# Kernel tuning notes

Measured on AMD Instinct MI355X. Metric: run time of the kernel, lower is better.

The kernel has to match this reference:

```python
import jax, jax.numpy as jnp
import numpy as np

COMMITMENT_COST = 0.25


def setup_inputs() -> dict:
    key = jax.random.key(0)
    k1, k2 = jax.random.split(key)
    x = jax.random.normal(k1, (32, 256, 32, 32), dtype=jnp.float32)          # NCHW latents
    embedding = jax.random.normal(k2, (1024, 256), dtype=jnp.float32)        # [K, D] codebook
    return {"x": x, "embedding": embedding}


def reference(x, embedding):
    # NCHW -> NHWC, flatten to [N, D]
    inp = jnp.transpose(x, (0, 2, 3, 1))
    B, H, W, D = inp.shape
    K = embedding.shape[0]
    flat = inp.reshape(-1, D)                                                # [N, D]

    dists = (jnp.sum(flat * flat, axis=1, keepdims=True)
             + jnp.sum(embedding * embedding, axis=1)
             - 2.0 * flat @ embedding.T)
    idx = jnp.argmin(dists, axis=1)                                          # [N]
    encodings = jax.nn.one_hot(idx, K, dtype=flat.dtype)                     # [N, K]

    quantized = (encodings @ embedding).reshape(B, H, W, D)

    # commitment loss (codebook detached, eval path: no EMA update)
    e_latent_loss = jnp.mean(jnp.square(jax.lax.stop_gradient(quantized) - inp))
    loss = COMMITMENT_COST * e_latent_loss

    # straight-through estimator
    quantized_st = inp + jax.lax.stop_gradient(quantized - inp)

    avg_probs = jnp.mean(encodings, axis=0)
    perplexity = jnp.exp(-jnp.sum(avg_probs * jnp.log(avg_probs + 1e-10)))

    return (loss, jnp.transpose(quantized_st, (0, 3, 1, 2)), perplexity, encodings)
```

## Files before the change

### kernel.cpp

```cpp
#include <hip/hip_runtime.h>
#include <math.h>

#define D    256
#define K    1024
#define HWX  1024
#define NPTS 32768
#define PT   64
#define NPAIR 32

#define Q_OFF    1
#define PERP_OFF (1 + 8388608)
#define ENC_OFF  (2 + 8388608)

#define WS_FRAG_OFF 147456

typedef __attribute__((ext_vector_type(8))) short bf16x8;
typedef __attribute__((ext_vector_type(4))) float f32x4;
typedef __attribute__((ext_vector_type(2))) float f32x2;

__device__ __forceinline__ unsigned short bf16_rne(float f) {
  unsigned int u = __float_as_uint(f);
  u = u + 0x7fffu + ((u >> 16) & 1u);
  return (unsigned short)(u >> 16);
}

#define CONV(F, H, L)                                                          \
  {                                                                            \
    H = bf16_rne(F);                                                           \
    const float fh_ = __uint_as_float((unsigned)(H) << 16);                    \
    L = bf16_rne((F)-fh_);                                                     \
  }

__global__ __launch_bounds__(256) void vq_frag(const float* __restrict__ emb,
                                               unsigned int* __restrict__ frag,
                                               float* __restrict__ enorm,
                                               int* __restrict__ counts,
                                               float* __restrict__ loss_accum) {
  const int gid = blockIdx.x * 256 + threadIdx.x;
  const int c = gid >> 5, g = gid & 31;
  const float* src = emb + (size_t)c * D + g * 8;
  const float4 a = *(const float4*)src;
  const float4 b = *(const float4*)(src + 4);
  float s = a.x * a.x + a.y * a.y + a.z * a.z + a.w * a.w +
            b.x * b.x + b.y * b.y + b.z * b.z + b.w * b.w;
#pragma unroll
  for (int off = 1; off < 32; off <<= 1) s += __shfl_xor(s, off);
  if (g == 0) enorm[c] = s;
  unsigned short h0, h1, h2, h3, h4, h5, h6, h7;
  unsigned short l0, l1, l2, l3, l4, l5, l6, l7;
  CONV(a.x, h0, l0) CONV(a.y, h1, l1) CONV(a.z, h2, l2) CONV(a.w, h3, l3)
  CONV(b.x, h4, l4) CONV(b.y, h5, l5) CONV(b.z, h6, l6) CONV(b.w, h7, l7)
  uint4 uh, ul;
  uh.x = (unsigned)h0 | ((unsigned)h1 << 16); uh.y = (unsigned)h2 | ((unsigned)h3 << 16);
  uh.z = (unsigned)h4 | ((unsigned)h5 << 16); uh.w = (unsigned)h6 | ((unsigned)h7 << 16);
  ul.x = (unsigned)l0 | ((unsigned)l1 << 16); ul.y = (unsigned)l2 | ((unsigned)l3 << 16);
  ul.z = (unsigned)l4 | ((unsigned)l5 << 16); ul.w = (unsigned)l6 | ((unsigned)l7 << 16);
  const int fragidx = (c >> 4) * 16 + (g >> 2) * 2;
  const int Lo = ((c & 15) + 16 * (g & 3)) * 4;
  *(uint4*)(frag + (size_t)fragidx * 256 + Lo) = uh;
  *(uint4*)(frag + (size_t)(fragidx + 1) * 256 + Lo) = ul;
  if (gid < K) counts[gid] = 0;
  if (gid == 0) *loss_accum = 0.0f;
}

#define ISSUE_PAIR(P, HALF)                                                    \
  {                                                                            \
    const unsigned* gsrc = fragg + (size_t)(P)*8192 + t * 4;                   \
    unsigned short* ldst = fbuf + (HALF)*16384 + t * 8;                        \
    _Pragma("unroll") for (int q = 0; q < 8; ++q)                              \
        __builtin_amdgcn_global_load_lds(                                      \
            (const __attribute__((address_space(1))) unsigned*)(gsrc + q * 1024), \
            (__attribute__((address_space(3))) unsigned*)(ldst + q * 2048),    \
            16, 0, 0);                                                         \
  }

#define AHOIST(KSv)                                                            \
  ah##KSv = *(const bf16x8*)&fbuf[((w * 4 + ((KSv)&3)) * 2 + 0) * 512 + lane * 8]; \
  al##KSv = *(const bf16x8*)&fbuf[((w * 4 + ((KSv)&3)) * 2 + 1) * 512 + lane * 8];

#define KS3G(KSv, ACC, BUFO)                                                   \
  {                                                                            \
    const bf16x8 bh = *(const bf16x8*)&fbuf[(BUFO) + ((KSv)*2 + 0) * 512 + lane * 8]; \
    const bf16x8 bl = *(const bf16x8*)&fbuf[(BUFO) + ((KSv)*2 + 1) * 512 + lane * 8]; \
    ACC = __builtin_amdgcn_mfma_f32_16x16x32_bf16(ah##KSv, bh, ACC, 0, 0, 0);  \
    ACC = __builtin_amdgcn_mfma_f32_16x16x32_bf16(al##KSv, bh, ACC, 0, 0, 0);  \
    ACC = __builtin_amdgcn_mfma_f32_16x16x32_bf16(ah##KSv, bl, ACC, 0, 0, 0);  \
  }

#define COMPUTE_PAIR(I)                                                        \
  {                                                                            \
    const int b0 = ((I)&1) * 16384;                                            \
    const int b1 = b0 + 8192;                                                  \
    f32x4 acc0 = {0.f, 0.f, 0.f, 0.f};                                         \
    f32x4 acc1 = {0.f, 0.f, 0.f, 0.f};                                         \
    KS3G(0, acc0, b0) KS3G(0, acc1, b1)                                        \
    KS3G(1, acc0, b0) KS3G(1, acc1, b1)                                        \
    KS3G(2, acc0, b0) KS3G(2, acc1, b1)                                        \
    KS3G(3, acc0, b0) KS3G(3, acc1, b1)                                        \
    KS3G(4, acc0, b0) KS3G(4, acc1, b1)                                        \
    KS3G(5, acc0, b0) KS3G(5, acc1, b1)                                        \
    KS3G(6, acc0, b0) KS3G(6, acc1, b1)                                        \
    KS3G(7, acc0, b0) KS3G(7, acc1, b1)                                        \
    const int c0 = (I)*32 + (lane & 15);                                       \
    const int c1 = c0 + 16;                                                    \
    const float e0 = en_s[c0], e1 = en_s[c1];                                  \
    float m;                                                                   \
    m = e0 - 2.0f * acc0[0]; if (m < mv[0]) { mv[0] = m; mi[0] = c0; }         \
    m = e0 - 2.0f * acc0[1]; if (m < mv[1]) { mv[1] = m; mi[1] = c0; }         \
    m = e0 - 2.0f * acc0[2]; if (m < mv[2]) { mv[2] = m; mi[2] = c0; }         \
    m = e0 - 2.0f * acc0[3]; if (m < mv[3]) { mv[3] = m; mi[3] = c0; }         \
    m = e1 - 2.0f * acc1[0]; if (m < mv[0]) { mv[0] = m; mi[0] = c1; }         \
    m = e1 - 2.0f * acc1[1]; if (m < mv[1]) { mv[1] = m; mi[1] = c1; }         \
    m = e1 - 2.0f * acc1[2]; if (m < mv[2]) { mv[2] = m; mi[2] = c1; }         \
    m = e1 - 2.0f * acc1[3]; if (m < mv[3]) { mv[3] = m; mi[3] = c1; }         \
  }

#define ENC_ZERO2(I)                                                           \
  {                                                                            \
    const f32x2 z_ = {0.f, 0.f};                                               \
    __builtin_nontemporal_store(z_, encz + (I)*1024 + t);                      \
    __builtin_nontemporal_store(z_, encz + (I)*1024 + 256 + t);                \
    __builtin_nontemporal_store(z_, encz + (I)*1024 + 512 + t);                \
    __builtin_nontemporal_store(z_, encz + (I)*1024 + 768 + t);                \
  }

#define CFENCE asm volatile("" ::: "memory");

#define STAGE_X(H)                                                             \
  {                                                                            \
    const int pt = t & 63, cb_ = t >> 6;                                       \
    const float* xb = x + (size_t)bb * (D * HWX) + hw0 + pt;                   \
    _Pragma("unroll 8") for (int i = 0; i < 32; ++i) {                         \
      const int c = (H)*128 + cb_ + 4 * i;                                     \
      const float f = xb[(size_t)c * HWX];                                     \
      unsigned short h_, l_;                                                   \
      CONV(f, h_, l_)                                                          \
      xn_acc += f * f;                                                         \
      const int ksl = (c >> 5) & 3, quad = (c >> 3) & 3, j = c & 7;            \
      const int base =                                                         \
          (((pt >> 4) * 4 + ksl) * 2) * 512 + ((pt & 15) + 16 * quad) * 8 + j; \
      fbuf[base] = h_;                                                         \
      fbuf[base + 512] = l_;                                                   \
    }                                                                          \
  }

__global__ __launch_bounds__(256) void vq_main(const float* __restrict__ x,
                                               const unsigned int* __restrict__ fragg,
                                               const float* __restrict__ emb,
                                               const float* __restrict__ enorm,
                                               float* __restrict__ out_q,
                                               float* __restrict__ out_enc,
                                               float* __restrict__ loss_accum,
                                               int* __restrict__ counts) {
  __shared__ __align__(16) unsigned short fbuf[32768];
  __shared__ float en_s[K];
  __shared__ float xn_part[256];
  __shared__ float val_s[PT];
  __shared__ int idx_s[PT];

  const int t = threadIdx.x;
  const int lane = t & 63;
  const int w = t >> 6;
  const int p0 = blockIdx.x * PT;
  const int bb = p0 >> 10;
  const int hw0 = p0 & 1023;

  bf16x8 ah0, ah1, ah2, ah3, ah4, ah5, ah6, ah7;
  bf16x8 al0, al1, al2, al3, al4, al5, al6, al7;
  float xn_acc = 0.0f;

  STAGE_X(0)
  for (int i = t; i < K; i += 256) en_s[i] = enorm[i];
  __syncthreads();
  AHOIST(0) AHOIST(1) AHOIST(2) AHOIST(3)
  __syncthreads();
  STAGE_X(1)
  xn_part[t] = xn_acc;
  __syncthreads();
  AHOIST(4) AHOIST(5) AHOIST(6) AHOIST(7)
  __syncthreads();

  float mv[4];
  int mi[4];
#pragma unroll
  for (int i = 0; i < 4; ++i) { mv[i] = 3.4e38f; mi[i] = 0; }

  f32x2* encz = reinterpret_cast<f32x2*>(out_enc + (size_t)p0 * K);

  ISSUE_PAIR(0, 0)
  asm volatile("s_waitcnt vmcnt(0)" ::: "memory");
  __builtin_amdgcn_s_barrier();
  for (int i = 0; i < NPAIR - 1; ++i) {
    CFENCE
    ISSUE_PAIR(i + 1, (i + 1) & 1)
    CFENCE
    ENC_ZERO2(i)
    CFENCE
    COMPUTE_PAIR(i)
    asm volatile("s_waitcnt vmcnt(4)" ::: "memory");
    __builtin_amdgcn_s_barrier();
  }
  CFENCE
  ENC_ZERO2(NPAIR - 1)
  COMPUTE_PAIR(NPAIR - 1)

#pragma unroll
  for (int off = 1; off < 16; off <<= 1) {
#pragma unroll
    for (int i = 0; i < 4; ++i) {
      const float ov = __shfl_xor(mv[i], off);
      const int oi = __shfl_xor(mi[i], off);
      if (ov < mv[i] || (ov == mv[i] && oi < mi[i])) { mv[i] = ov; mi[i] = oi; }
    }
  }
  if ((lane & 15) == 0) {
    const int quad = lane >> 4;
#pragma unroll
    for (int i = 0; i < 4; ++i) {
      val_s[w * 16 + quad * 4 + i] = mv[i];
      idx_s[w * 16 + quad * 4 + i] = mi[i];
    }
  }
  asm volatile("s_waitcnt vmcnt(0)" ::: "memory");
  __syncthreads();

  float dist = 0.0f;
  if (t < PT) {
    float xn = 0.0f;
#pragma unroll
    for (int g = 0; g < 4; ++g) xn += xn_part[t + 64 * g];
    dist = val_s[t] + xn;
    atomicAdd(&counts[idx_s[t]], 1);
    out_enc[(size_t)(p0 + t) * K + idx_s[t]] = 1.0f;
  }
  if (t < 64) {
#pragma unroll
    for (int off = 32; off > 0; off >>= 1) dist += __shfl_down(dist, off);
    if (t == 0) atomicAdd(loss_accum, dist);
  }

  float* xq = (float*)fbuf;
  for (int qd = 0; qd < 4; ++qd) {
    __syncthreads();
#pragma unroll
    for (int rr = 0; rr < 4; ++rr) {
      const int r = w * 4 + rr;
      const float4 v = ((const float4*)(emb + (size_t)idx_s[qd * 16 + r] * D))[lane];
      float* dst = &xq[r * 257 + lane];
      dst[0] = v.x; dst[64] = v.y; dst[128] = v.z; dst[192] = v.w;
    }
    __syncthreads();
    const int pt = t & 15;
    float* qb = out_q + (size_t)bb * D * HWX + hw0 + qd * 16 + pt;
#pragma unroll
    for (int ii = 0; ii < 16; ++ii) {
      const int ci = (t >> 4) + 16 * ii;
      const int pos = (ci >> 2) + 64 * (ci & 3);
      qb[(size_t)ci * HWX] = xq[pt * 257 + pos];
    }
  }
}

__global__ __launch_bounds__(256) void vq_final(const int* __restrict__ counts,
                                                const float* __restrict__ loss_accum,
                                                float* __restrict__ out) {
  __shared__ float sh[4];
  const int t = threadIdx.x;
  float s = 0.0f;
  for (int k = t; k < K; k += 256) {
    const float p = (float)counts[k] * (1.0f / 32768.0f);
    s += p * logf(p + 1e-10f);
  }
#pragma unroll
  for (int off = 32; off > 0; off >>= 1) s += __shfl_down(s, off);
  if ((t & 63) == 0) sh[t >> 6] = s;
  __syncthreads();
  if (t == 0) {
    const float tot = sh[0] + sh[1] + sh[2] + sh[3];
    out[PERP_OFF] = expf(-tot);
    out[0] = 0.25f * (*loss_accum) / 8388608.0f;
  }
}

extern "C" void kernel_launch(void* const* d_in, const int* in_sizes, int n_in,
                              void* d_out, int out_size, void* d_ws, size_t ws_size,
                              hipStream_t stream) {
  const float* x = (const float*)d_in[0];
  const float* emb = (const float*)d_in[1];
  float* out = (float*)d_out;
  float* enorm = (float*)d_ws;
  int* counts = (int*)((char*)d_ws + 4096);
  float* loss_accum = (float*)((char*)d_ws + 8192);
  unsigned int* fragg = (unsigned int*)((char*)d_ws + WS_FRAG_OFF);

  hipLaunchKernelGGL(vq_frag, dim3(128), dim3(256), 0, stream,
                     emb, fragg, enorm, counts, loss_accum);
  hipLaunchKernelGGL(vq_main, dim3(NPTS / PT), dim3(256), 0, stream,
                     x, fragg, emb, enorm, out + Q_OFF, out + ENC_OFF,
                     loss_accum, counts);
  hipLaunchKernelGGL(vq_final, dim3(1), dim3(256), 0, stream,
                     counts, loss_accum, out);
}
```

Before: 249.6 us.

## Fuse final reduction via last-block ticket, stage x in one pass, add MFMA priority

Removes the separate vq_final launch by having the last block to finish, chosen with an atomic ticket, compute perplexity and loss. It also stages all 256 input channels into LDS in a single pass, which drops two barriers and changes the A-fragment layout to match. MFMA sections are wrapped in s_setprio to favour matrix issue. The costs are an extra atomic and fence per block, plus a possible LDS layout mismatch if the new layout is inconsistent with the tile size.

```diff
diff --git a/kernel.cpp b/kernel.cpp
--- a/kernel.cpp
+++ b/kernel.cpp
@@ -35,7 +35,8 @@
                                                unsigned int* __restrict__ frag,
                                                float* __restrict__ enorm,
                                                int* __restrict__ counts,
-                                               float* __restrict__ loss_accum) {
+                                               float* __restrict__ loss_accum,
+                                               unsigned int* __restrict__ ticket) {
   const int gid = blockIdx.x * 256 + threadIdx.x;
   const int c = gid >> 5, g = gid & 31;
   const float* src = emb + (size_t)c * D + g * 8;
@@ -60,7 +61,7 @@
   *(uint4*)(frag + (size_t)fragidx * 256 + Lo) = uh;
   *(uint4*)(frag + (size_t)(fragidx + 1) * 256 + Lo) = ul;
   if (gid < K) counts[gid] = 0;
-  if (gid == 0) *loss_accum = 0.0f;
+  if (gid == 0) { *loss_accum = 0.0f; *ticket = 0u; }
 }
 
 #define ISSUE_PAIR(P, HALF)                                                    \
@@ -75,8 +76,8 @@
   }
 
 #define AHOIST(KSv)                                                            \
-  ah##KSv = *(const bf16x8*)&fbuf[((w * 4 + ((KSv)&3)) * 2 + 0) * 512 + lane * 8]; \
-  al##KSv = *(const bf16x8*)&fbuf[((w * 4 + ((KSv)&3)) * 2 + 1) * 512 + lane * 8];
+  ah##KSv = *(const bf16x8*)&fbuf[((w * 8 + (KSv)) * 2 + 0) * 512 + lane * 8]; \
+  al##KSv = *(const bf16x8*)&fbuf[((w * 8 + (KSv)) * 2 + 1) * 512 + lane * 8];
 
 #define KS3G(KSv, ACC, BUFO)                                                   \
   {                                                                            \
@@ -93,6 +94,7 @@
     const int b1 = b0 + 8192;                                                  \
     f32x4 acc0 = {0.f, 0.f, 0.f, 0.f};                                         \
     f32x4 acc1 = {0.f, 0.f, 0.f, 0.f};                                         \
+    __builtin_amdgcn_s_setprio(1);                                             \
     KS3G(0, acc0, b0) KS3G(0, acc1, b1)                                        \
     KS3G(1, acc0, b0) KS3G(1, acc1, b1)                                        \
     KS3G(2, acc0, b0) KS3G(2, acc1, b1)                                        \
@@ -101,6 +103,7 @@
     KS3G(5, acc0, b0) KS3G(5, acc1, b1)                                        \
     KS3G(6, acc0, b0) KS3G(6, acc1, b1)                                        \
     KS3G(7, acc0, b0) KS3G(7, acc1, b1)                                        \
+    __builtin_amdgcn_s_setprio(0);                                             \
     const int c0 = (I)*32 + (lane & 15);                                       \
     const int c1 = c0 + 16;                                                    \
     const float e0 = en_s[c0], e1 = en_s[c1];                                  \
@@ -126,37 +129,23 @@
 
 #define CFENCE asm volatile("" ::: "memory");
 
-#define STAGE_X(H)                                                             \
-  {                                                                            \
-    const int pt = t & 63, cb_ = t >> 6;                                       \
-    const float* xb = x + (size_t)bb * (D * HWX) + hw0 + pt;                   \
-    _Pragma("unroll 8") for (int i = 0; i < 32; ++i) {                         \
-      const int c = (H)*128 + cb_ + 4 * i;                                     \
-      const float f = xb[(size_t)c * HWX];                                     \
-      unsigned short h_, l_;                                                   \
-      CONV(f, h_, l_)                                                          \
-      xn_acc += f * f;                                                         \
-      const int ksl = (c >> 5) & 3, quad = (c >> 3) & 3, j = c & 7;            \
-      const int base =                                                         \
-          (((pt >> 4) * 4 + ksl) * 2) * 512 + ((pt & 15) + 16 * quad) * 8 + j; \
-      fbuf[base] = h_;                                                         \
-      fbuf[base + 512] = l_;                                                   \
-    }                                                                          \
-  }
-
 __global__ __launch_bounds__(256) void vq_main(const float* __restrict__ x,
                                                const unsigned int* __restrict__ fragg,
                                                const float* __restrict__ emb,
                                                const float* __restrict__ enorm,
-                                               float* __restrict__ out_q,
-                                               float* __restrict__ out_enc,
+                                               float* __restrict__ out,
                                                float* __restrict__ loss_accum,
-                                               int* __restrict__ counts) {
+                                               int* __restrict__ counts,
+                                               unsigned int* __restrict__ ticket) {
   __shared__ __align__(16) unsigned short fbuf[32768];
   __shared__ float en_s[K];
   __shared__ float xn_part[256];
   __shared__ float val_s[PT];
   __shared__ int idx_s[PT];
+  __shared__ unsigned int rank_s;
+
+  float* out_q = out + Q_OFF;
+  float* out_enc = out + ENC_OFF;
 
   const int t = threadIdx.x;
   const int lane = t & 63;
@@ -169,14 +158,27 @@
   bf16x8 al0, al1, al2, al3, al4, al5, al6, al7;
   float xn_acc = 0.0f;
 
-  STAGE_X(0)
+  {
+    const int pt = t & 63, cb_ = t >> 6;
+    const float* xb = x + (size_t)bb * (D * HWX) + hw0 + pt;
+#pragma unroll 8
+    for (int i = 0; i < 64; ++i) {
+      const int c = cb_ + 4 * i;
+      const float f = xb[(size_t)c * HWX];
+      unsigned short h_, l_;
+      CONV(f, h_, l_)
+      xn_acc += f * f;
+      const int ks = c >> 5, quad = (c >> 3) & 3, j = c & 7;
+      const int base =
+          (((pt >> 4) * 8 + ks) * 2) * 512 + ((pt & 15) + 16 * quad) * 8 + j;
+      fbuf[base] = h_;
+      fbuf[base + 512] = l_;
+    }
+  }
   for (int i = t; i < K; i += 256) en_s[i] = enorm[i];
+  xn_part[t] = xn_acc;
   __syncthreads();
   AHOIST(0) AHOIST(1) AHOIST(2) AHOIST(3)
-  __syncthreads();
-  STAGE_X(1)
-  xn_part[t] = xn_acc;
-  __syncthreads();
   AHOIST(4) AHOIST(5) AHOIST(6) AHOIST(7)
   __syncthreads();
 
@@ -259,26 +261,34 @@
       qb[(size_t)ci * HWX] = xq[pt * 257 + pos];
     }
   }
-}
-
-__global__ __launch_bounds__(256) void vq_final(const int* __restrict__ counts,
-                                                const float* __restrict__ loss_accum,
-                                                float* __restrict__ out) {
-  __shared__ float sh[4];
-  const int t = threadIdx.x;
-  float s = 0.0f;
-  for (int k = t; k < K; k += 256) {
-    const float p = (float)counts[k] * (1.0f / 32768.0f);
-    s += p * logf(p + 1e-10f);
-  }
-#pragma unroll
-  for (int off = 32; off > 0; off >>= 1) s += __shfl_down(s, off);
-  if ((t & 63) == 0) sh[t >> 6] = s;
+
+  asm volatile("s_waitcnt vmcnt(0)" ::: "memory");
   __syncthreads();
   if (t == 0) {
-    const float tot = sh[0] + sh[1] + sh[2] + sh[3];
-    out[PERP_OFF] = expf(-tot);
-    out[0] = 0.25f * (*loss_accum) / 8388608.0f;
+    __threadfence();
+    rank_s = atomicAdd(ticket, 1u);
+  }
+  __syncthreads();
+  if (rank_s == (unsigned)(NPTS / PT) - 1u) {
+    __threadfence();
+    float s = 0.0f;
+    for (int k = t; k < K; k += 256) {
+      const int c = __hip_atomic_load(&counts[k], __ATOMIC_RELAXED,
+                                      __HIP_MEMORY_SCOPE_AGENT);
+      const float p = (float)c * (1.0f / 32768.0f);
+      s += p * logf(p + 1e-10f);
+    }
+#pragma unroll
+    for (int off = 32; off > 0; off >>= 1) s += __shfl_down(s, off);
+    if (lane == 0) val_s[w] = s;
+    __syncthreads();
+    if (t == 0) {
+      const float tot = val_s[0] + val_s[1] + val_s[2] + val_s[3];
+      const float loss = __hip_atomic_load(loss_accum, __ATOMIC_RELAXED,
+                                           __HIP_MEMORY_SCOPE_AGENT);
+      out[PERP_OFF] = expf(-tot);
+      out[0] = 0.25f * loss / 8388608.0f;
+    }
   }
 }
 
@@ -291,13 +301,11 @@
   float* enorm = (float*)d_ws;
   int* counts = (int*)((char*)d_ws + 4096);
   float* loss_accum = (float*)((char*)d_ws + 8192);
+  unsigned int* ticket = (unsigned int*)((char*)d_ws + 8200);
   unsigned int* fragg = (unsigned int*)((char*)d_ws + WS_FRAG_OFF);
 
   hipLaunchKernelGGL(vq_frag, dim3(128), dim3(256), 0, stream,
-                     emb, fragg, enorm, counts, loss_accum);
+                     emb, fragg, enorm, counts, loss_accum, ticket);
   hipLaunchKernelGGL(vq_main, dim3(NPTS / PT), dim3(256), 0, stream,
-                     x, fragg, emb, enorm, out + Q_OFF, out + ENC_OFF,
-                     loss_accum, counts);
-  hipLaunchKernelGGL(vq_final, dim3(1), dim3(256), 0, stream,
-                     counts, loss_accum, out);
+                     x, fragg, emb, enorm, out, loss_accum, counts, ticket);
 }
```

Measured after the change: 272.5 us. +9.2%, slower.
